# Kernel tuning notes

Measured on AMD Instinct MI355X. Metric: run time of the kernel, lower is better.

Reference implementation:

```python
import jax, jax.numpy as jnp
import numpy as np

NUM_EMBEDDINGS = 512
EMBEDDING_DIM = 64
DECAY = 0.995
EXPECTED_COUNT = 1024 * 16 * 16 / NUM_EMBEDDINGS  # batch_size * H * W / K = 512.0


def setup_inputs() -> dict:
    key = jax.random.key(0)
    k1, k2 = jax.random.split(key)
    z_e = jax.random.normal(k1, (1024, EMBEDDING_DIM, 16, 16), dtype=jnp.float32)
    e = jax.random.normal(k2, (NUM_EMBEDDINGS, EMBEDDING_DIM), dtype=jnp.float32)
    N = jnp.ones((NUM_EMBEDDINGS,), dtype=jnp.float32) * EXPECTED_COUNT
    return {"z_e": z_e, "e": e, "N": N}


def reference(z_e, e, N):
    B, D, H, W = z_e.shape
    # (B, D, H, W) -> (B*H*W, D)
    z_flat = jnp.transpose(z_e, (0, 2, 3, 1)).reshape(-1, D)
    # squared euclidean distances: ||z||^2 + ||e||^2 - 2 z.e^T  -> [B*H*W, K]
    dist = (
        jnp.sum(z_flat * z_flat, axis=1, keepdims=True)
        + jnp.sum(e * e, axis=1)[None, :]
        - 2.0 * (z_flat @ e.T)
    )
    indices_flat = jnp.argmin(dist, axis=1)
    # embedding gather, back to (B, D, H, W)
    z_q = e[indices_flat].reshape(B, H, W, D)
    z_q = jnp.transpose(z_q, (0, 3, 1, 2))
    # training-mode EMA bincount update of cluster counts
    n_i = jnp.zeros((e.shape[0],), dtype=jnp.float32).at[indices_flat].add(1.0)
    N_new = DECAY * N + (1.0 - DECAY) * n_i
    return z_q, N_new
```

## Files before the change

### kernel.cpp

```cpp
#include <hip/hip_runtime.h>

#define KCODES 512
#define DIM    64
#define PXB    512
#define NCT    32
#define MARGIN 0.125f

typedef __attribute__((ext_vector_type(8))) short        short8;
typedef __attribute__((ext_vector_type(8))) _Float16     half8;
typedef __attribute__((ext_vector_type(4))) float        floatx4;
typedef __attribute__((ext_vector_type(2))) unsigned int uint2v;

__device__ __host__ inline int sigma_dim(int p) {
    return ((p >> 5) << 5) + (((p >> 2) & 1) << 4) + (((p >> 3) & 3) << 2) + (p & 3);
}

__global__ __launch_bounds__(256) void vq_setup(const float* __restrict__ e,
        float* __restrict__ enorm, _Float16* __restrict__ ehf,
        float* __restrict__ counts, unsigned* __restrict__ tick)
{
    const int tg = blockIdx.x * 256 + threadIdx.x;
    const int c = tg >> 6, j = tg & 63;
    const int g = j >> 3, i = j & 7;
    const int gs = g ^ (c & 7);
    const int dsrc = sigma_dim(gs * 8 + i);
    ehf[tg] = (_Float16)(-2.f * e[c * DIM + dsrc]);
    if (tg < KCODES) {
        const float* er = e + tg * DIM;
        float s = 0.f;
        #pragma unroll
        for (int d = 0; d < DIM; ++d) s = fmaf(er[d], er[d], s);
        enorm[tg]  = s;
        counts[tg] = 0.f;
        if (tg == 0) *tick = 0u;
    }
}

__device__ inline unsigned mono(float f) {
    unsigned u = __float_as_uint(f);
    return (u & 0x80000000u) ? ~u : (u | 0x80000000u);
}
__device__ inline float unmono(unsigned u) {
    return __uint_as_float((u & 0x80000000u) ? (u & 0x7FFFFFFFu) : ~u);
}

#define DPP64(dst, src, CTRL) {                                                       \
    int _lo = __builtin_amdgcn_update_dpp(0, (int)(unsigned)((src) & 0xFFFFFFFFull),  \
                                          CTRL, 0xF, 0xF, true);                      \
    int _hi = __builtin_amdgcn_update_dpp(0, (int)(unsigned)((src) >> 32),            \
                                          CTRL, 0xF, 0xF, true);                      \
    dst = (((unsigned long long)(unsigned)_hi) << 32) | (unsigned)_lo; }

#define MERGE_STEP(CTRL) {                                                            \
    unsigned long long o1, o2; DPP64(o1, k1, CTRL); DPP64(o2, k2, CTRL);              \
    unsigned long long mx  = k1 > o1 ? k1 : o1;                                       \
    unsigned long long mn2 = k2 < o2 ? k2 : o2;                                       \
    k1 = k1 < o1 ? k1 : o1;                                                           \
    k2 = mx < mn2 ? mx : mn2; }

__global__ __launch_bounds__(1024, 8) void vq_main(
        const float* __restrict__ z, const float* __restrict__ e,
        const _Float16* __restrict__ ehf, const float* __restrict__ enorm,
        const float* __restrict__ N, float* __restrict__ zq,
        float* __restrict__ counts, unsigned* __restrict__ tick,
        float* __restrict__ outN)
{
    __shared__ __align__(16) _Float16 S[KCODES * DIM];
    __shared__ float ens[KCODES];
    __shared__ int   hist[KCODES];
    __shared__ int   idxs[PXB];
    __shared__ int   ref2[PXB];
    __shared__ int   lastflag;

    const int t    = threadIdx.x;
    const int b    = blockIdx.x;
    const int lane = t & 63;
    const int wave = t >> 6;
    const int n16  = lane & 15;
    const int g4   = lane >> 4;

    if (t < KCODES) { ens[t] = enorm[t]; hist[t] = 0; }

    {
        float4 v[8];
        #pragma unroll
        for (int i = 0; i < 8; ++i) {
            const int L  = i * 1024 + t;
            const int bb = L >> 12, d = (L >> 6) & 63, c4 = L & 63;
            v[i] = *(const float4*)(z + (size_t)((b * 2 + bb) * DIM + d) * 256 + c4 * 4);
        }
        #pragma unroll
        for (int i = 0; i < 8; ++i) {
            const int L  = i * 1024 + t;
            const int bb = L >> 12, d = (L >> 6) & 63, c4 = L & 63;
            union { _Float16 h[4]; uint2v u; } pk;
            pk.h[0] = (_Float16)v[i].x; pk.h[1] = (_Float16)v[i].y;
            pk.h[2] = (_Float16)v[i].z; pk.h[3] = (_Float16)v[i].w;
            const int chunk = bb * 16 + (c4 >> 2);
            *(uint2v*)(S + chunk * 1024 + d * 16 + (c4 & 3) * 4) = pk.u;
        }
    }
    __syncthreads();

    half8 A[2][2];
    {
        uint2v r[2][2][2];
        const int trb = n16 * 2 + g4 * 128;
        #pragma unroll
        for (int pt = 0; pt < 2; ++pt) {
            const int base = (wave * 2 + pt) * 2048 + trb;
            #pragma unroll
            for (int ks = 0; ks < 2; ++ks) {
                const int a0 = base + ks * 1024;
                asm volatile("ds_read_b64_tr_b16 %0, %1" : "=v"(r[pt][ks][0]) : "v"(a0));
                asm volatile("ds_read_b64_tr_b16 %0, %1" : "=v"(r[pt][ks][1]) : "v"(a0 + 512));
            }
        }
        asm volatile("s_waitcnt lgkmcnt(0)" ::: "memory");
        __builtin_amdgcn_sched_barrier(0);
        #pragma unroll
        for (int pt = 0; pt < 2; ++pt)
            #pragma unroll
            for (int ks = 0; ks < 2; ++ks) {
                union { unsigned int u[4]; half8 h; } pk;
                pk.u[0] = r[pt][ks][0].x; pk.u[1] = r[pt][ks][0].y;
                pk.u[2] = r[pt][ks][1].x; pk.u[3] = r[pt][ks][1].y;
                A[pt][ks] = pk.h;
            }
    }
    __syncthreads();

    {
        const short8* src = (const short8*)ehf;
        short8* dst = (short8*)S;
        #pragma unroll
        for (int k = 0; k < 4; ++k)
            dst[t + k * 1024] = src[t + k * 1024];
    }
    __syncthreads();

    const int xr = n16 & 7;
    const int byte0 = n16 * 128 + (((g4    ) ^ xr) << 4);
    const int byte1 = n16 * 128 + (((4 | g4) ^ xr) << 4);
    const char* hb = (const char*)S;

    float bestv[2][4];
    int   bct[2][4];
    #pragma unroll
    for (int pt = 0; pt < 2; ++pt)
        #pragma unroll
        for (int r = 0; r < 4; ++r) { bestv[pt][r] = 3.4e38f; bct[pt][r] = 0; }

    #pragma unroll 2
    for (int ct = 0; ct < NCT; ++ct) {
        const int cb = ct * 2048;
        half8 B0 = *(const half8*)(hb + cb + byte0);
        half8 B1 = *(const half8*)(hb + cb + byte1);
        const float en = ens[ct * 16 + n16];
        #pragma unroll
        for (int pt = 0; pt < 2; ++pt) {
            floatx4 C = {en, en, en, en};
            C = __builtin_amdgcn_mfma_f32_16x16x32_f16(A[pt][0], B0, C, 0, 0, 0);
            C = __builtin_amdgcn_mfma_f32_16x16x32_f16(A[pt][1], B1, C, 0, 0, 0);
            #pragma unroll
            for (int r = 0; r < 4; ++r) {
                float s = C[r];
                if (s < bestv[pt][r]) { bestv[pt][r] = s; bct[pt][r] = ct; }
            }
        }
    }

    #pragma unroll
    for (int pt = 0; pt < 2; ++pt)
        #pragma unroll
        for (int r = 0; r < 4; ++r) {
            unsigned long long k1 =
                (((unsigned long long)mono(bestv[pt][r])) << 32)
                | (unsigned)(bct[pt][r] * 16 + n16);
            unsigned long long k2 = ~0ull;
            MERGE_STEP(0xB1);
            MERGE_STEP(0x4E);
            MERGE_STEP(0x124);
            MERGE_STEP(0x128);
            if (n16 == 0) {
                const int px = wave * 32 + pt * 16 + g4 * 4 + r;
                const float f1 = unmono((unsigned)(k1 >> 32));
                const float f2 = unmono((unsigned)(k2 >> 32));
                idxs[px] = (int)(k1 & 0xFFFFFFFFull);
                ref2[px] = (f2 - f1 < MARGIN) ? (int)(k2 & 0xFFFFFFFFull) : -1;
            }
        }

    __syncthreads();

    if (t < PXB) {
        int bi = idxs[t];
        const int r2 = ref2[t];
        if (r2 >= 0) {
            const int gp = b * PXB + t;
            const int bb = gp >> 8, hw = gp & 255;
            const float* zb = z + (size_t)bb * (DIM * 256) + hw;
            const float* e1 = e + bi * DIM;
            const float* e2 = e + r2 * DIM;
            float d1 = 0.f, d2 = 0.f;
            #pragma unroll
            for (int d = 0; d < DIM; ++d) {
                const float zd = zb[(size_t)d * 256];
                d1 = fmaf(zd, e1[d], d1);
                d2 = fmaf(zd, e2[d], d2);
            }
            const float s1 = fmaf(-2.f, d1, ens[bi]);
            const float s2 = fmaf(-2.f, d2, ens[r2]);
            if (s2 < s1 || (s2 == s1 && r2 < bi)) bi = r2;
            idxs[t] = bi;
        }
        atomicAdd(&hist[bi], 1);
    }
    __syncthreads();

    if (t < KCODES) { int h = hist[t]; if (h) atomicAdd(&counts[t], (float)h); }
    __syncthreads();
    if (t == 0) {
        __threadfence();
        unsigned o = __hip_atomic_fetch_add(tick, 1u, __ATOMIC_ACQ_REL,
                                            __HIP_MEMORY_SCOPE_AGENT);
        lastflag = (o == gridDim.x - 1u);
    }
    __syncthreads();

    {
        const int px = t & 511, dh = (t >> 9) * 32;
        const int bi = idxs[px];
        const int gp = b * PXB + px;
        const int bb = gp >> 8, hw = gp & 255;
        const float4* er4 = (const float4*)(e + bi * DIM + dh);
        float* ob = zq + (size_t)bb * (DIM * 256) + (size_t)dh * 256 + hw;
        #pragma unroll
        for (int q = 0; q < 8; ++q) {
            float4 v = er4[q];
            ob[(size_t)(4 * q + 0) * 256] = v.x;
            ob[(size_t)(4 * q + 1) * 256] = v.y;
            ob[(size_t)(4 * q + 2) * 256] = v.z;
            ob[(size_t)(4 * q + 3) * 256] = v.w;
        }
    }

    if (lastflag && t < KCODES) {
        float c = __hip_atomic_load(&counts[t], __ATOMIC_RELAXED,
                                    __HIP_MEMORY_SCOPE_AGENT);
        outN[t] = 0.995f * N[t] + 0.005f * c;
    }
}

extern "C" void kernel_launch(void* const* d_in, const int* in_sizes, int n_in,
                              void* d_out, int out_size, void* d_ws, size_t ws_size,
                              hipStream_t stream) {
    const float* z = (const float*)d_in[0];
    const float* e = (const float*)d_in[1];
    const float* N = (const float*)d_in[2];
    float* out = (float*)d_out;
    const int nz     = in_sizes[0];
    const int npix   = nz / DIM;
    const int blocks = npix / PXB;

    char* ws = (char*)d_ws;
    float*     enorm  = (float*)(ws);
    float*     counts = (float*)(ws + 2048);
    unsigned*  tick   = (unsigned*)(ws + 4096);
    _Float16*  ehf    = (_Float16*)(ws + 4352);

    vq_setup<<<(KCODES * DIM) / 256, 256, 0, stream>>>(e, enorm, ehf, counts, tick);
    vq_main<<<blocks, 1024, 0, stream>>>(z, e, ehf, enorm, N, out, counts,
                                         tick, out + nz);
}
```

Baseline: 167.7 us.

## Halve block to one image per block and prefetch codebook into registers early

Each block now processes 256 pixels (one image) with 512 threads instead of 512 pixels with 1024 threads, doubling the grid and simplifying addressing. The fp16 codebook load from global memory is issued alongside the z loads into registers before the first barrier, so its latency overlaps with the z staging instead of being a separate serialized phase. The trade-off is higher register use per thread (eight short8 values held live) and twice as many blocks repeating the per-block codebook copy into shared memory, counts atomics and tick increment.

After: 204.2 us. 21.7% more time.

```diff
diff --git a/kernel.cpp b/kernel.cpp
--- a/kernel.cpp
+++ b/kernel.cpp
@@ -2,7 +2,7 @@
 
 #define KCODES 512
 #define DIM    64
-#define PXB    512
+#define PXB    256
 #define NCT    32
 #define MARGIN 0.125f
 
@@ -58,7 +58,7 @@
     k1 = k1 < o1 ? k1 : o1;                                                           \
     k2 = mx < mn2 ? mx : mn2; }
 
-__global__ __launch_bounds__(1024, 8) void vq_main(
+__global__ __launch_bounds__(512, 4) void vq_main(
         const float* __restrict__ z, const float* __restrict__ e,
         const _Float16* __restrict__ ehf, const float* __restrict__ enorm,
         const float* __restrict__ N, float* __restrict__ zq,
@@ -79,26 +79,30 @@
     const int n16  = lane & 15;
     const int g4   = lane >> 4;
 
-    if (t < KCODES) { ens[t] = enorm[t]; hist[t] = 0; }
-
-    {
-        float4 v[8];
-        #pragma unroll
-        for (int i = 0; i < 8; ++i) {
-            const int L  = i * 1024 + t;
-            const int bb = L >> 12, d = (L >> 6) & 63, c4 = L & 63;
-            v[i] = *(const float4*)(z + (size_t)((b * 2 + bb) * DIM + d) * 256 + c4 * 4);
-        }
-        #pragma unroll
-        for (int i = 0; i < 8; ++i) {
-            const int L  = i * 1024 + t;
-            const int bb = L >> 12, d = (L >> 6) & 63, c4 = L & 63;
-            union { _Float16 h[4]; uint2v u; } pk;
-            pk.h[0] = (_Float16)v[i].x; pk.h[1] = (_Float16)v[i].y;
-            pk.h[2] = (_Float16)v[i].z; pk.h[3] = (_Float16)v[i].w;
-            const int chunk = bb * 16 + (c4 >> 2);
-            *(uint2v*)(S + chunk * 1024 + d * 16 + (c4 & 3) * 4) = pk.u;
-        }
+    ens[t] = enorm[t]; hist[t] = 0;
+
+    const float* zimg = z + (size_t)b * (DIM * 256);
+    float4 v[8];
+    #pragma unroll
+    for (int i = 0; i < 8; ++i) {
+        const int d   = (wave + (i & 1) * 8) * 4 + g4;
+        const int px4 = (i >> 1) * 16 + n16;
+        v[i] = *(const float4*)(zimg + (size_t)d * 256 + px4 * 4);
+    }
+    short8 ev[8];
+    {
+        const short8* src = (const short8*)ehf;
+        #pragma unroll
+        for (int k = 0; k < 8; ++k) ev[k] = src[t + k * 512];
+    }
+    #pragma unroll
+    for (int i = 0; i < 8; ++i) {
+        const int d   = (wave + (i & 1) * 8) * 4 + g4;
+        const int px4 = (i >> 1) * 16 + n16;
+        union { _Float16 h[4]; uint2v u; } pk;
+        pk.h[0] = (_Float16)v[i].x; pk.h[1] = (_Float16)v[i].y;
+        pk.h[2] = (_Float16)v[i].z; pk.h[3] = (_Float16)v[i].w;
+        *(uint2v*)(S + (px4 >> 2) * 1024 + d * 16 + (px4 & 3) * 4) = pk.u;
     }
     __syncthreads();
 
@@ -131,11 +135,10 @@
     __syncthreads();
 
     {
-        const short8* src = (const short8*)ehf;
         short8* dst = (short8*)S;
         #pragma unroll
-        for (int k = 0; k < 4; ++k)
-            dst[t + k * 1024] = src[t + k * 1024];
+        for (int k = 0; k < 8; ++k)
+            dst[t + k * 512] = ev[k];
     }
     __syncthreads();
 
@@ -197,9 +200,7 @@
         int bi = idxs[t];
         const int r2 = ref2[t];
         if (r2 >= 0) {
-            const int gp = b * PXB + t;
-            const int bb = gp >> 8, hw = gp & 255;
-            const float* zb = z + (size_t)bb * (DIM * 256) + hw;
+            const float* zb = zimg + t;
             const float* e1 = e + bi * DIM;
             const float* e2 = e + r2 * DIM;
             float d1 = 0.f, d2 = 0.f;
@@ -218,7 +219,7 @@
     }
     __syncthreads();
 
-    if (t < KCODES) { int h = hist[t]; if (h) atomicAdd(&counts[t], (float)h); }
+    { int h = hist[t]; if (h) atomicAdd(&counts[t], (float)h); }
     __syncthreads();
     if (t == 0) {
         __threadfence();
@@ -229,23 +230,21 @@
     __syncthreads();
 
     {
-        const int px = t & 511, dh = (t >> 9) * 32;
+        const int px = t & 255, dh = (t >> 8) * 32;
         const int bi = idxs[px];
-        const int gp = b * PXB + px;
-        const int bb = gp >> 8, hw = gp & 255;
         const float4* er4 = (const float4*)(e + bi * DIM + dh);
-        float* ob = zq + (size_t)bb * (DIM * 256) + (size_t)dh * 256 + hw;
+        float* ob = zq + (size_t)b * (DIM * 256) + (size_t)dh * 256 + px;
         #pragma unroll
         for (int q = 0; q < 8; ++q) {
-            float4 v = er4[q];
-            ob[(size_t)(4 * q + 0) * 256] = v.x;
-            ob[(size_t)(4 * q + 1) * 256] = v.y;
-            ob[(size_t)(4 * q + 2) * 256] = v.z;
-            ob[(size_t)(4 * q + 3) * 256] = v.w;
-        }
-    }
-
-    if (lastflag && t < KCODES) {
+            float4 w = er4[q];
+            ob[(size_t)(4 * q + 0) * 256] = w.x;
+            ob[(size_t)(4 * q + 1) * 256] = w.y;
+            ob[(size_t)(4 * q + 2) * 256] = w.z;
+            ob[(size_t)(4 * q + 3) * 256] = w.w;
+        }
+    }
+
+    if (lastflag) {
         float c = __hip_atomic_load(&counts[t], __ATOMIC_RELAXED,
                                     __HIP_MEMORY_SCOPE_AGENT);
         outN[t] = 0.995f * N[t] + 0.005f * c;
@@ -270,6 +269,6 @@
     _Float16*  ehf    = (_Float16*)(ws + 4352);
 
     vq_setup<<<(KCODES * DIM) / 256, 256, 0, stream>>>(e, enorm, ehf, counts, tick);
-    vq_main<<<blocks, 1024, 0, stream>>>(z, e, ehf, enorm, N, out, counts,
-                                         tick, out + nz);
-}
+    vq_main<<<blocks, 512, 0, stream>>>(z, e, ehf, enorm, N, out, counts,
+                                        tick, out + nz);
+}
```
